# Performance work log

Measured on AMD Instinct MI355X. Metric: run time of the kernel, lower is better.

Reference implementation:

```python
import jax, jax.numpy as jnp
import numpy as np

DIM = 768
NUM_HEADS = 12
HEAD_DIM = DIM // NUM_HEADS
SCALE = HEAD_DIM ** -0.5
SPARSITY = 0.1


def setup_inputs() -> dict:
    key = jax.random.key(0)
    ks = jax.random.split(key, 6)
    B, N, C = 2, 4096, DIM
    s = 0.02
    return {
        "x": jax.random.normal(ks[0], (B, N, C), dtype=jnp.float32),
        "Wq": jax.random.normal(ks[1], (C, C), dtype=jnp.float32) * s,
        "Wk": jax.random.normal(ks[2], (C, C), dtype=jnp.float32) * s,
        "Wv": jax.random.normal(ks[3], (C, C), dtype=jnp.float32) * s,
        "Wp": jax.random.normal(ks[4], (C, C), dtype=jnp.float32) * s,
        "bp": jax.random.normal(ks[5], (C,), dtype=jnp.float32) * s,
    }


def reference(x, Wq, Wk, Wv, Wp, bp):
    B, N, C = x.shape
    H, D = NUM_HEADS, HEAD_DIM
    # nn.Linear: y = x @ W.T ; here W is stored as (out, in) equivalent -> use W.T
    q = (x @ Wq.T).reshape(B, N, H, D).transpose(0, 2, 1, 3)  # [B,H,N,D]
    k = (x @ Wk.T).reshape(B, N, H, D).transpose(0, 2, 1, 3)
    v = (x @ Wv.T).reshape(B, N, H, D).transpose(0, 2, 1, 3)
    attn = jnp.einsum("bhnd,bhmd->bhnm", q, k) * SCALE  # [B,H,N,N]
    attn = jax.nn.softmax(attn, axis=-1)
    num_keep = max(1, int(N * SPARSITY))
    topk_vals, topk_idx = jax.lax.top_k(attn, num_keep)  # [B,H,N,K]
    bi = jnp.arange(B)[:, None, None, None]
    hi = jnp.arange(H)[None, :, None, None]
    ni = jnp.arange(N)[None, None, :, None]
    sparse_attn = jnp.zeros_like(attn).at[bi, hi, ni, topk_idx].set(topk_vals)
    out = jnp.einsum("bhnm,bhmd->bhnd", sparse_attn, v)  # [B,H,N,D]
    out = out.transpose(0, 2, 1, 3).reshape(B, N, C)
    return out @ Wp.T + bp
```

## Files before the change

kernel.cpp:

```cpp
#include <hip/hip_runtime.h>


typedef unsigned short u16;
typedef unsigned int   u32;
typedef float    f32x4 __attribute__((ext_vector_type(4)));
typedef _Float16 f16x8 __attribute__((ext_vector_type(8)));
typedef u16      u16x8 __attribute__((ext_vector_type(8)));
typedef u16      u16x4 __attribute__((ext_vector_type(4)));
typedef u32      u32x4 __attribute__((ext_vector_type(4)));

#define NHEADS 12
#define SEQ    4096
#define DIMC   768
#define HDIM   64
#define KKEEP  409

__device__ __forceinline__ f32x4 mfma16(f16x8 a, f16x8 b, f32x4 c) {
  return __builtin_amdgcn_mfma_f32_16x16x32_f16(a, b, c, 0, 0, 0);
}
__device__ __forceinline__ u16 f2h_bits(float f) {
  return __builtin_bit_cast(u16, (_Float16)f);
}
__device__ __forceinline__ float h2f_bits(u16 b) {
  return (float)__builtin_bit_cast(_Float16, b);
}

__device__ __forceinline__ u32 wred_add_u32(u32 x) {
  x += (u32)__builtin_amdgcn_update_dpp(0, (int)x, 0x111, 0xF, 0xF, true);
  x += (u32)__builtin_amdgcn_update_dpp(0, (int)x, 0x112, 0xF, 0xF, true);
  x += (u32)__builtin_amdgcn_update_dpp(0, (int)x, 0x114, 0xF, 0xF, true);
  x += (u32)__builtin_amdgcn_update_dpp(0, (int)x, 0x118, 0xF, 0xF, true);
  x += (u32)__builtin_amdgcn_update_dpp(0, (int)x, 0x142, 0xF, 0xF, true);
  x += (u32)__builtin_amdgcn_update_dpp(0, (int)x, 0x143, 0xF, 0xF, true);
  return (u32)__builtin_amdgcn_readlane((int)x, 63);
}
__device__ __forceinline__ float wred_add_f32(float x) {
#define _DPPF(ctrl) x += __builtin_bit_cast(float, __builtin_amdgcn_update_dpp( \
      0, __builtin_bit_cast(int, x), ctrl, 0xF, 0xF, true));
  _DPPF(0x111) _DPPF(0x112) _DPPF(0x114) _DPPF(0x118) _DPPF(0x142) _DPPF(0x143)
#undef _DPPF
  return __builtin_bit_cast(float, __builtin_amdgcn_readlane(__builtin_bit_cast(int, x), 63));
}
__device__ __forceinline__ u32 wred_min_u32(u32 x) {
#define _DPPM(ctrl) { u32 y = (u32)__builtin_amdgcn_update_dpp((int)0xFFFFFFFF, (int)x, ctrl, 0xF, 0xF, false); \
                      x = x < y ? x : y; }
  _DPPM(0x111) _DPPM(0x112) _DPPM(0x114) _DPPM(0x118) _DPPM(0x142) _DPPM(0x143)
#undef _DPPM
  return (u32)__builtin_amdgcn_readlane((int)x, 63);
}

__global__ __launch_bounds__(256) void cast_f32_to_f16(const float* __restrict__ in,
                                                       u16* __restrict__ out, int n4) {
  int i = blockIdx.x * 256 + threadIdx.x;
  if (i >= n4) return;
  float4 v = ((const float4*)in)[i];
  u16x4 o;
  o[0] = f2h_bits(v.x); o[1] = f2h_bits(v.y); o[2] = f2h_bits(v.z); o[3] = f2h_bits(v.w);
  ((u16x4*)out)[i] = o;
}

template<int MODE>
__global__ __launch_bounds__(256) void gemm_nt(const u16* __restrict__ A, const u16* __restrict__ B,
                                               float scale, const float* __restrict__ bias,
                                               void* __restrict__ dstv) {
  __shared__ __align__(16) u16 As[128 * 64];
  __shared__ __align__(16) u16 Bs[128 * 64];
  const int tid  = threadIdx.x;
  const int lane = tid & 63, wave = tid >> 6;
  const int l15 = lane & 15, l4 = lane >> 4;
  const int row0 = blockIdx.x * 128, col0 = blockIdx.y * 128;
  const int wr = (wave >> 1) * 64, wc = (wave & 1) * 64;
  f32x4 acc[4][4];
#pragma unroll
  for (int i = 0; i < 4; i++)
#pragma unroll
    for (int j = 0; j < 4; j++) acc[i][j] = f32x4{0.f, 0.f, 0.f, 0.f};

  for (int k0 = 0; k0 < DIMC; k0 += 64) {
#pragma unroll
    for (int i = 0; i < 4; i++) {
      int id = tid + i * 256;
      int r = id >> 3, c = id & 7;
      f16x8 va = *(const f16x8*)(A + (size_t)(row0 + r) * DIMC + k0 + c * 8);
      f16x8 vb = *(const f16x8*)(B + (size_t)(col0 + r) * DIMC + k0 + c * 8);
      *(f16x8*)(As + r * 64 + ((c ^ (r & 7)) << 3)) = va;
      *(f16x8*)(Bs + r * 64 + ((c ^ (r & 7)) << 3)) = vb;
    }
    __syncthreads();
#pragma unroll
    for (int ks = 0; ks < 2; ++ks) {
      f16x8 af[4], bfr[4];
#pragma unroll
      for (int i = 0; i < 4; i++) {
        int r = wr + i * 16 + l15;
        int c = ks * 4 + l4;
        af[i] = *(const f16x8*)(As + r * 64 + ((c ^ (r & 7)) << 3));
        int r2 = wc + i * 16 + l15;
        bfr[i] = *(const f16x8*)(Bs + r2 * 64 + ((c ^ (r2 & 7)) << 3));
      }
#pragma unroll
      for (int i = 0; i < 4; i++)
#pragma unroll
        for (int j = 0; j < 4; j++) acc[i][j] = mfma16(af[i], bfr[j], acc[i][j]);
    }
    __syncthreads();
  }

#pragma unroll
  for (int i = 0; i < 4; i++) {
#pragma unroll
    for (int j = 0; j < 4; j++) {
      int rowb = row0 + wr + i * 16 + (l4 << 2);
      int col  = col0 + wc + j * 16 + l15;
      if (MODE == 2) {
        float* dst = (float*)dstv;
        float bv = bias[col];
#pragma unroll
        for (int jj = 0; jj < 4; jj++)
          dst[(size_t)(rowb + jj) * DIMC + col] = acc[i][j][jj] + bv;
      } else if (MODE == 0) {
        u16* dst = (u16*)dstv;
        int hh = col >> 6, d = col & 63;
#pragma unroll
        for (int jj = 0; jj < 4; jj++) {
          int row = rowb + jj;
          int bb = row >> 12, n = row & 4095;
          dst[(((size_t)bb * NHEADS + hh) * SEQ + n) * HDIM + d] = f2h_bits(acc[i][j][jj] * scale);
        }
      } else {
        u16* dst = (u16*)dstv;
        int hh = col >> 6, d = col & 63;
        int bb = rowb >> 12, nb = rowb & 4095;
        u16x4 pack;
#pragma unroll
        for (int jj = 0; jj < 4; jj++) pack[jj] = f2h_bits(acc[i][j][jj] * scale);
        *(u16x4*)(dst + (((size_t)bb * NHEADS + hh) * HDIM + d) * SEQ + nb) = pack;
      }
    }
  }
}

__global__ __launch_bounds__(256) void qk_exp(const u16* __restrict__ Q, const u16* __restrict__ K,
                                              u16* __restrict__ P, int bh0) {
  __shared__ __align__(16) u16 bounce[4][32 * 128];
  const int tid = threadIdx.x, lane = tid & 63, wave = tid >> 6;
  const int l15 = lane & 15, l4 = lane >> 4;
  const size_t bhg = (size_t)bh0 + blockIdx.z;
  const int q0 = blockIdx.x * 128 + wave * 32;
  const int k0 = blockIdx.y * 128;
  const u16* Qh = Q + (bhg * SEQ + q0) * HDIM;
  const u16* Kh = K + (bhg * SEQ + k0) * HDIM;

  f16x8 qf[2][2];
#pragma unroll
  for (int qr = 0; qr < 2; ++qr)
#pragma unroll
    for (int kh = 0; kh < 2; ++kh)
      qf[qr][kh] = *(const f16x8*)(Qh + (qr * 16 + l15) * HDIM + kh * 32 + l4 * 8);

  u16* bw = bounce[wave];
#pragma unroll 2
  for (int ks = 0; ks < 8; ++ks) {
    const u16* kp = Kh + (size_t)(ks * 16 + l15) * HDIM + l4 * 8;
    f16x8 kf0 = *(const f16x8*)kp;
    f16x8 kf1 = *(const f16x8*)(kp + 32);
#pragma unroll
    for (int qr = 0; qr < 2; ++qr) {
      f32x4 acc = f32x4{0.f, 0.f, 0.f, 0.f};
      acc = mfma16(kf0, qf[qr][0], acc);
      acc = mfma16(kf1, qf[qr][1], acc);
      int row = qr * 16 + l15;
      int gran = ks * 2 + (l4 >> 1);
      u16x4 pack;
#pragma unroll
      for (int j = 0; j < 4; j++) pack[j] = f2h_bits(__expf(fminf(acc[j], 11.0f)));
      *(u16x4*)(bw + row * 128 + ((gran ^ (row & 7)) << 3) + ((l4 & 1) << 2)) = pack;
    }
  }
  __syncthreads();
#pragma unroll
  for (int R = 0; R < 8; ++R) {
    int row = R * 4 + (lane >> 4);
    int gran = lane & 15;
    f16x8 v = *(const f16x8*)(bw + row * 128 + ((gran ^ (row & 7)) << 3));
    *(f16x8*)(P + ((size_t)blockIdx.z * SEQ + q0 + row) * SEQ + k0 + gran * 8) = v;
  }
}

__global__ __launch_bounds__(512) void select_rows(const u16* __restrict__ P, u32* __restrict__ meta) {
  const int tid = threadIdx.x, lane = tid & 63, wave = tid >> 6;
  const size_t row = (size_t)blockIdx.x * 8 + wave;
  const u16* Pr = P + row * SEQ;
  const u32 H = 0x80008000u;
  u32 X[8][4];
#pragma unroll
  for (int cc = 0; cc < 8; ++cc) {
    u32x4 v = *(const u32x4*)(Pr + cc * 512 + lane * 8);
#pragma unroll
    for (int p = 0; p < 4; p++) X[cc][p] = v[p] | H;
  }
  float z = 0.f;
#pragma unroll
  for (int cc = 0; cc < 8; ++cc)
#pragma unroll
    for (int p = 0; p < 4; p++) {
      u32 x = X[cc][p];
      z += h2f_bits((u16)(x & 0x7FFFu));
      z += h2f_bits((u16)((x >> 16) & 0x7FFFu));
    }
  z = wred_add_f32(z);
  float invZ = 1.f / z;
  u32 lo = 0, hi = 0x7FFFu, c1 = 0;
  while (lo < hi) {
    u32 mid = (lo + hi) >> 1;
    u32 M1 = (mid + 1) * 0x10001u;
    u32 pc = 0;
#pragma unroll
    for (int cc = 0; cc < 8; ++cc)
#pragma unroll
      for (int p = 0; p < 4; p++) {
        u32 d = X[cc][p] - M1;
        pc += (d & H) >> 15;
      }
    u32 s = wred_add_u32(pc);
    u32 cnt = (s & 0xFFFFu) + (s >> 16);
    if (cnt < KKEEP) { hi = mid; c1 = cnt; } else lo = mid + 1;
  }
  const u32 t = lo;
  const int r = KKEEP - (int)c1;
  const u32 M1t = (t + 1) * 0x10001u;
  const u32 M0t = t * 0x10001u;
  int run = 0; u32 cstar = 0;
  for (int cc = 0; cc < 8; ++cc) {
    u32 eqm[4]; u32 s = 0;
#pragma unroll
    for (int p = 0; p < 4; p++) {
      u32 x = X[cc][p];
      u32 g1 = (x - M1t) & H;
      u32 g0 = (x - M0t) & H;
      eqm[p] = g0 ^ g1;
      s += eqm[p] >> 15;
    }
    int ec = (int)((s & 0xFFFFu) + (s >> 16));
    int inc = ec;
#pragma unroll
    for (int o = 1; o < 64; o <<= 1) { int pf = __shfl_up(inc, o); if (lane >= o) inc += pf; }
    int tot = __shfl(inc, 63);
    if (run + tot >= r) {
      int need = r - run;
      int local = need - (inc - ec);
      u32 cand = 0xFFFFFFFFu; int cnt2 = 0;
#pragma unroll
      for (int p = 0; p < 4; p++)
#pragma unroll
        for (int half = 0; half < 2; half++) {
          u32 eq = half ? (eqm[p] >> 31) : ((eqm[p] >> 15) & 1u);
          if (eq) { cnt2++; if (cnt2 == local) cand = (u32)(cc * 512 + lane * 8 + p * 2 + half); }
        }
      cstar = wred_min_u32(cand);
      break;
    }
    run += tot;
  }
  if (lane == 0) {
    u32x4 m; m[0] = t; m[1] = cstar; m[2] = __builtin_bit_cast(u32, invZ); m[3] = 0;
    *(u32x4*)(meta + row * 4) = m;
  }
}

__global__ __launch_bounds__(512, 4) void pv_apply(const u16* __restrict__ P, const u32* __restrict__ meta,
                                                   const u16* __restrict__ Vt, u16* __restrict__ Ob, int bh0) {
  __shared__ float Opart[8][16][65];
  __shared__ u32 smeta[16][3];
  const int tid = threadIdx.x, lane = tid & 63, wave = tid >> 6;
  const int l15 = lane & 15, l4 = lane >> 4;
  const int bhl = blockIdx.y;
  const int bhg = bh0 + bhl;
  const int b = bhg / NHEADS, h = bhg - b * NHEADS;
  const int r0 = blockIdx.x * 16;
  const u16* Pbh = P + (size_t)bhl * SEQ * SEQ;
  const u16* Vh  = Vt + (size_t)bhg * HDIM * SEQ;
  const u32 H = 0x80008000u;

  if (tid < 16) {
    u32x4 m = *(const u32x4*)(meta + ((size_t)bhl * SEQ + r0 + tid) * 4);
    smeta[tid][0] = m[0]; smeta[tid][1] = m[1]; smeta[tid][2] = m[2];
  }
  __syncthreads();

  const u32 t = smeta[l15][0];
  const int cstar = (int)smeta[l15][1];
  const u32 Mt = t * 0x10001u;
  const u16* Prow = Pbh + (size_t)(r0 + l15) * SEQ + wave * 512 + l4 * 8;
  f32x4 acc[4];
#pragma unroll
  for (int ds = 0; ds < 4; ds++) acc[ds] = f32x4{0.f, 0.f, 0.f, 0.f};
#pragma unroll 2
  for (int kb = 0; kb < 512; kb += 32) {
    u32x4 praw = *(const u32x4*)(Prow + kb);
    int base = cstar - (wave * 512 + kb + l4 * 8);
    u32x4 om;
#pragma unroll
    for (int p = 0; p < 4; ++p) {
      u32 s0 = (u32)(base - 2 * p) >> 31;
      u32 s1 = (u32)(base - 2 * p - 1) >> 31;
      u32 M1 = Mt + s0 + (s1 << 16);
      u32 d  = (praw[p] | H) - M1;
      u32 g  = d & H;
      u32 m  = g | (g - (g >> 15));
      om[p]  = praw[p] & m;
    }
    f16x8 pb = __builtin_bit_cast(f16x8, om);
#pragma unroll
    for (int ds = 0; ds < 4; ++ds) {
      f16x8 af = *(const f16x8*)(Vh + (size_t)(ds * 16 + l15) * SEQ + wave * 512 + kb + l4 * 8);
      acc[ds] = mfma16(af, pb, acc[ds]);
    }
  }
#pragma unroll
  for (int ds = 0; ds < 4; ++ds)
#pragma unroll
    for (int j = 0; j < 4; j++)
      Opart[wave][l15][ds * 16 + l4 * 4 + j] = acc[ds][j];
  __syncthreads();
#pragma unroll
  for (int i = tid; i < 16 * 64; i += 512) {
    int row = i >> 6, d = i & 63;
    float v = 0.f;
#pragma unroll
    for (int w = 0; w < 8; ++w) v += Opart[w][row][d];
    v *= __builtin_bit_cast(float, smeta[row][2]);
    Ob[((size_t)b * SEQ + r0 + row) * DIMC + h * HDIM + d] = f2h_bits(v);
  }
}

extern "C" void kernel_launch(void* const* d_in, const int* in_sizes, int n_in,
                              void* d_out, int out_size, void* d_ws, size_t ws_size,
                              hipStream_t stream) {
  const float* x  = (const float*)d_in[0];
  const float* Wq = (const float*)d_in[1];
  const float* Wk = (const float*)d_in[2];
  const float* Wv = (const float*)d_in[3];
  const float* Wp = (const float*)d_in[4];
  const float* bp = (const float*)d_in[5];
  float* out = (float*)d_out;

  const size_t M = 2 * (size_t)SEQ;
  const size_t XB = M * DIMC * 2;
  const size_t WB = (size_t)DIMC * DIMC * 2;
  const size_t NBH = 2 * NHEADS;

  char* w = (char*)d_ws;
  u16* xb   = (u16*)w; w += XB;
  u16* Wqb  = (u16*)w; w += WB;
  u16* Wkb  = (u16*)w; w += WB;
  u16* Wvb  = (u16*)w; w += WB;
  u16* Wpb  = (u16*)w; w += WB;
  u16* Qb   = (u16*)w; w += XB;
  u16* Kbuf = (u16*)w; w += XB;
  u16* Vtb  = (u16*)w; w += XB;
  u16* Obuf = (u16*)w; w += XB;
  u32* meta = (u32*)w; w += NBH * SEQ * 16;
  u16* Pbuf = (u16*)w;

  size_t used  = (size_t)(w - (char*)d_ws);
  size_t avail = ws_size > used ? ws_size - used : 0;
  const size_t perBh = (size_t)SEQ * SEQ * 2;
  int chunk = (int)(avail / perBh);
  if (chunk > (int)NBH) chunk = (int)NBH;
  if (chunk < 1) chunk = 1;

  cast_f32_to_f16<<<6144, 256, 0, stream>>>(x,  xb,  (int)(M * DIMC / 4));
  cast_f32_to_f16<<<576,  256, 0, stream>>>(Wq, Wqb, (int)(WB / 8));
  cast_f32_to_f16<<<576,  256, 0, stream>>>(Wk, Wkb, (int)(WB / 8));
  cast_f32_to_f16<<<576,  256, 0, stream>>>(Wv, Wvb, (int)(WB / 8));
  cast_f32_to_f16<<<576,  256, 0, stream>>>(Wp, Wpb, (int)(WB / 8));

  dim3 gg(64, 6);
  gemm_nt<0><<<gg, 256, 0, stream>>>(xb, Wqb, 0.125f, nullptr, Qb);
  gemm_nt<0><<<gg, 256, 0, stream>>>(xb, Wkb, 1.0f,   nullptr, Kbuf);
  gemm_nt<1><<<gg, 256, 0, stream>>>(xb, Wvb, 1.0f,   nullptr, Vtb);

  for (int bh0 = 0; bh0 < (int)NBH; bh0 += chunk) {
    int nb = (int)NBH - bh0; if (nb > chunk) nb = chunk;
    qk_exp     <<<dim3(32, 32, nb), 256, 0, stream>>>(Qb, Kbuf, Pbuf, bh0);
    select_rows<<<dim3(nb * 512),   512, 0, stream>>>(Pbuf, meta);
    pv_apply   <<<dim3(256, nb),    512, 0, stream>>>(Pbuf, meta, Vtb, Obuf, bh0);
  }

  gemm_nt<2><<<gg, 256, 0, stream>>>(Obuf, Wpb, 1.0f, bp, out);
}
```

Baseline: 1.157 ms.

## Stage P tiles through swizzled LDS with register prefetch in pv_apply

The P row loads in pv_apply used to be strided per lane, with 16 rows each read as 16-byte fragments. They now become coalesced row-contiguous global loads of 512-column chunks, written into a swizzled LDS buffer that reuses the Opart storage. The next chunk is prefetched into registers while the current one is consumed. Each wave now covers a 64-column slice of every chunk, not a 512-column span, and the change adds two block barriers per chunk. The aim is better global coalescing for the large P read, paid for with extra synchronisation and LDS traffic.

```diff
diff --git a/kernel.cpp b/kernel.cpp
--- a/kernel.cpp
+++ b/kernel.cpp
@@ -270,7 +270,9 @@
 
 __global__ __launch_bounds__(512, 4) void pv_apply(const u16* __restrict__ P, const u32* __restrict__ meta,
                                                    const u16* __restrict__ Vt, u16* __restrict__ Ob, int bh0) {
-  __shared__ float Opart[8][16][65];
+  __shared__ __align__(16) char lds_raw[8 * 16 * 65 * 4];
+  u16*  Pst   = (u16*)lds_raw;
+  float* Opf  = (float*)lds_raw;
   __shared__ u32 smeta[16][3];
   const int tid = threadIdx.x, lane = tid & 63, wave = tid >> 6;
   const int l15 = lane & 15, l4 = lane >> 4;
@@ -286,49 +288,73 @@
     u32x4 m = *(const u32x4*)(meta + ((size_t)bhl * SEQ + r0 + tid) * 4);
     smeta[tid][0] = m[0]; smeta[tid][1] = m[1]; smeta[tid][2] = m[2];
   }
+
+  const int srow = tid >> 5, skg = (tid & 31) * 2;
+  const u16* Pg = Pbh + (size_t)(r0 + srow) * SEQ + skg * 8;
+  u16* sd0 = Pst + srow * 520 + ((skg ^ (srow & 7)) << 3);
+  u16* sd1 = Pst + srow * 520 + (((skg + 1) ^ (srow & 7)) << 3);
+
+  u32x4 g0 = *(const u32x4*)(Pg);
+  u32x4 g1 = *(const u32x4*)(Pg + 8);
+
   __syncthreads();
-
   const u32 t = smeta[l15][0];
   const int cstar = (int)smeta[l15][1];
   const u32 Mt = t * 0x10001u;
-  const u16* Prow = Pbh + (size_t)(r0 + l15) * SEQ + wave * 512 + l4 * 8;
+
   f32x4 acc[4];
 #pragma unroll
   for (int ds = 0; ds < 4; ds++) acc[ds] = f32x4{0.f, 0.f, 0.f, 0.f};
-#pragma unroll 2
-  for (int kb = 0; kb < 512; kb += 32) {
-    u32x4 praw = *(const u32x4*)(Prow + kb);
-    int base = cstar - (wave * 512 + kb + l4 * 8);
-    u32x4 om;
-#pragma unroll
-    for (int p = 0; p < 4; ++p) {
-      u32 s0 = (u32)(base - 2 * p) >> 31;
-      u32 s1 = (u32)(base - 2 * p - 1) >> 31;
-      u32 M1 = Mt + s0 + (s1 << 16);
-      u32 d  = (praw[p] | H) - M1;
-      u32 g  = d & H;
-      u32 m  = g | (g - (g >> 15));
-      om[p]  = praw[p] & m;
-    }
-    f16x8 pb = __builtin_bit_cast(f16x8, om);
-#pragma unroll
-    for (int ds = 0; ds < 4; ++ds) {
-      f16x8 af = *(const f16x8*)(Vh + (size_t)(ds * 16 + l15) * SEQ + wave * 512 + kb + l4 * 8);
-      acc[ds] = mfma16(af, pb, acc[ds]);
-    }
-  }
+
+#pragma unroll 1
+  for (int kc = 0; kc < 8; ++kc) {
+    *(u32x4*)sd0 = g0;
+    *(u32x4*)sd1 = g1;
+    __syncthreads();
+    if (kc < 7) {
+      g0 = *(const u32x4*)(Pg + (kc + 1) * 512);
+      g1 = *(const u32x4*)(Pg + (kc + 1) * 512 + 8);
+    }
+#pragma unroll
+    for (int it = 0; it < 2; ++it) {
+      const int kbl = wave * 64 + it * 32;
+      const int kg = (kbl >> 3) + l4;
+      u32x4 praw = *(const u32x4*)(Pst + l15 * 520 + ((kg ^ (l15 & 7)) << 3));
+      const int gk = kc * 512 + kbl + l4 * 8;
+      int base = cstar - gk;
+      u32x4 om;
+#pragma unroll
+      for (int p = 0; p < 4; ++p) {
+        u32 s0 = (u32)(base - 2 * p) >> 31;
+        u32 s1 = (u32)(base - 2 * p - 1) >> 31;
+        u32 M1 = Mt + s0 + (s1 << 16);
+        u32 d  = (praw[p] | H) - M1;
+        u32 g  = d & H;
+        u32 m  = g | (g - (g >> 15));
+        om[p]  = praw[p] & m;
+      }
+      f16x8 pb = __builtin_bit_cast(f16x8, om);
+#pragma unroll
+      for (int ds = 0; ds < 4; ++ds) {
+        f16x8 af = *(const f16x8*)(Vh + (size_t)(ds * 16 + l15) * SEQ + kc * 512 + kbl + l4 * 8);
+        acc[ds] = mfma16(af, pb, acc[ds]);
+      }
+    }
+    __syncthreads();
+  }
+
 #pragma unroll
   for (int ds = 0; ds < 4; ++ds)
 #pragma unroll
     for (int j = 0; j < 4; j++)
-      Opart[wave][l15][ds * 16 + l4 * 4 + j] = acc[ds][j];
+      Opf[(wave * 16 + l15) * 65 + ds * 16 + l4 * 4 + j] = acc[ds][j];
   __syncthreads();
 #pragma unroll
   for (int i = tid; i < 16 * 64; i += 512) {
     int row = i >> 6, d = i & 63;
     float v = 0.f;
 #pragma unroll
-    for (int w = 0; w < 8; ++w) v += Opart[w][row][d];
+    for (int w = 0; w < 8; ++w) v += Opf[(w * 16 + row) * 65 + d];
     v *= __builtin_bit_cast(float, smeta[row][2]);
     Ob[((size_t)b * SEQ + r0 + row) * DIMC + h * HDIM + d] = f2h_bits(v);
   }
```

Result: faster. 1.132 ms (-2.1%).
